# Kernel optimization log

Hardware: AMD Instinct MI355X
Metric: run time of the kernel (lower is better)

Reference implementation:

```python
import jax, jax.numpy as jnp
import numpy as np

TOPK = 16  # module init arg
EPS = 1e-12  # F.normalize eps


def setup_inputs() -> dict:
    key = jax.random.key(0)
    k1, k2, k3 = jax.random.split(key, 3)
    b, c, h, w = 2, 256, 96, 96
    rc = max(c // 4, 16)  # reduced_channels = 64
    x = jax.random.normal(k1, (b, c, h, w), dtype=jnp.float32)
    # 1x1 convs are channel-mixing matmuls; store weights as [out_ch, in_ch]
    w_reduce = jax.random.normal(k2, (rc, c), dtype=jnp.float32) * 0.05
    w_proj = jax.random.normal(k3, (c, rc), dtype=jnp.float32) * 0.05
    return {"x": x, "w_reduce": w_reduce, "w_proj": w_proj}


def reference(x, w_reduce, w_proj):
    b, c, h, w = x.shape
    n = h * w
    # reduce: 1x1 conv == channel matmul -> [b, rc, N]
    feat = jnp.einsum('rc,bchw->brhw', w_reduce, x).reshape(b, -1, n)
    # F.normalize(dim=1): divide by max(L2-norm over channels, eps)
    nrm = jnp.maximum(jnp.sqrt(jnp.sum(feat * feat, axis=1, keepdims=True)), EPS)
    nf = jnp.transpose(feat / nrm, (0, 2, 1))  # [b, N, rc]
    # cosine similarity matrix [b, N, N]
    sim = jnp.einsum('bnr,bmr->bnm', nf, nf)
    k = min(TOPK, n)
    _, idx = jax.lax.top_k(sim, k)  # [b, N, k]
    # gather top-k neighbor features and average -> [b, N, rc]
    corr = jax.vmap(lambda f, i: f[i].mean(axis=1))(nf, idx)
    # proj: 1x1 conv back to C channels, NCHW layout
    enhanced = jnp.einsum('cr,bnr->bnc', w_proj, corr)
    enhanced = jnp.transpose(enhanced, (0, 2, 1)).reshape(b, c, h, w)
    return x + enhanced
```

## Files before the change

### kernel.cpp

```cpp
#include <hip/hip_runtime.h>
#include <cstdint>
#include <cstddef>

#define NPIX 9216
#define NB 2
#define NC 256
#define RC 64
#define TK 16
#define NROWS (NB * NPIX)
#define CT 128
#define ECOLS 1152
#define NTE 9
#define MAXC 128
#define MARGIN 0.008f

typedef unsigned short ushort_t;
typedef unsigned int uint_t;
typedef __bf16 bf16x8 __attribute__((ext_vector_type(8)));
typedef float f32x4 __attribute__((ext_vector_type(4)));

__device__ __forceinline__ uint_t f2bf(float x) {
  uint_t u = __float_as_uint(x);
  return (u + 0x7FFFu + ((u >> 16) & 1u)) >> 16;
}

__device__ __forceinline__ uint_t ordu(float v) {
  uint_t u = __float_as_uint(v);
  return (u & 0x80000000u) ? ~u : (u | 0x80000000u);
}

__global__ __launch_bounds__(256) void k_reduce(
    const float* __restrict__ x, const float* __restrict__ wr,
    float* __restrict__ feat4) {
  __shared__ float wl[64 * 16];
  const int bi = blockIdx.x;
  const int pg = bi >> 4, rq = (bi >> 2) & 3, cq = bi & 3;
  const int tid = threadIdx.x;
  {
    const int cl = tid >> 2, rg = (tid & 3) * 4;
#pragma unroll
    for (int i = 0; i < 4; ++i)
      wl[cl * 16 + rg + i] = wr[(size_t)(rq * 16 + rg + i) * NC + cq * 64 + cl];
  }
  __syncthreads();

  const int p = pg * 256 + tid;
  const int b = p >= NPIX;
  const int n = p - b * NPIX;
  const float* xp = x + (size_t)b * NC * NPIX + (size_t)cq * 64 * NPIX + n;

  float4 acc[4];
#pragma unroll
  for (int i = 0; i < 4; ++i) acc[i] = make_float4(0.f, 0.f, 0.f, 0.f);

  for (int c = 0; c < 64; ++c) {
    const float xv = xp[(size_t)c * NPIX];
    const float4* w4 = (const float4*)(wl + c * 16);
#pragma unroll
    for (int i = 0; i < 4; ++i) {
      float4 w = w4[i];
      acc[i].x += w.x * xv; acc[i].y += w.y * xv;
      acc[i].z += w.z * xv; acc[i].w += w.w * xv;
    }
  }
  float4* o = (float4*)(feat4 + (((size_t)(rq * 4 + cq)) * NROWS + p) * 16);
#pragma unroll
  for (int i = 0; i < 4; ++i) o[i] = acc[i];
}

__global__ __launch_bounds__(256) void k_normsplit(
    const float* __restrict__ feat4, float* __restrict__ nf,
    ushort_t* __restrict__ hi) {
  const int t = blockIdx.x * 256 + threadIdx.x;
  const int p = t >> 2, q = t & 3;
  float4 v[4];
#pragma unroll
  for (int i = 0; i < 4; ++i) v[i] = make_float4(0.f, 0.f, 0.f, 0.f);
#pragma unroll
  for (int pt = 0; pt < 4; ++pt) {
    const float4* fp = (const float4*)(feat4 + (((size_t)(q * 4 + pt)) * NROWS + p) * 16);
#pragma unroll
    for (int i = 0; i < 4; ++i) {
      float4 a = fp[i];
      v[i].x += a.x; v[i].y += a.y; v[i].z += a.z; v[i].w += a.w;
    }
  }
  float ssq = 0.f;
#pragma unroll
  for (int i = 0; i < 4; ++i)
    ssq += v[i].x * v[i].x + v[i].y * v[i].y + v[i].z * v[i].z + v[i].w * v[i].w;
  ssq += __shfl_xor(ssq, 1);
  ssq += __shfl_xor(ssq, 2);
  const float inv = 1.f / fmaxf(sqrtf(ssq), 1e-12f);

  float s[16];
#pragma unroll
  for (int i = 0; i < 4; ++i) {
    s[i * 4 + 0] = v[i].x * inv; s[i * 4 + 1] = v[i].y * inv;
    s[i * 4 + 2] = v[i].z * inv; s[i * 4 + 3] = v[i].w * inv;
  }
  float4* no = (float4*)(nf + (size_t)p * RC + q * 16);
#pragma unroll
  for (int i = 0; i < 4; ++i)
    no[i] = make_float4(s[i * 4], s[i * 4 + 1], s[i * 4 + 2], s[i * 4 + 3]);

  uint_t hs[16];
#pragma unroll
  for (int i = 0; i < 16; ++i) hs[i] = f2bf(s[i]);
  uint4* ho = (uint4*)(hi + (size_t)p * RC + q * 16);
#pragma unroll
  for (int h = 0; h < 2; ++h)
    ho[h] = make_uint4(hs[h*8+0] | (hs[h*8+1] << 16), hs[h*8+2] | (hs[h*8+3] << 16),
                       hs[h*8+4] | (hs[h*8+5] << 16), hs[h*8+6] | (hs[h*8+7] << 16));
}

__global__ __launch_bounds__(256) void k_sim_max(
    const ushort_t* __restrict__ nf_hi, float* __restrict__ tmax) {
  __shared__ ushort_t sh[CT * 72];
  const int rb = blockIdx.x >> 3, q = blockIdx.x & 7;
  const int tid = threadIdx.x, wave = tid >> 6, lane = tid & 63;
  const int n = lane & 15, quad = lane >> 4;
  const int r0 = rb * 128 + wave * 32 + n, r1 = r0 + 16;
  const int b = rb >= 72;
  const size_t cbase = (size_t)b * NPIX;

  const bf16x8 bh00 = *(const bf16x8*)(nf_hi + (size_t)r0 * 64 + quad * 8);
  const bf16x8 bh01 = *(const bf16x8*)(nf_hi + (size_t)r0 * 64 + 32 + quad * 8);
  const bf16x8 bh10 = *(const bf16x8*)(nf_hi + (size_t)r1 * 64 + quad * 8);
  const bf16x8 bh11 = *(const bf16x8*)(nf_hi + (size_t)r1 * 64 + 32 + quad * 8);

  const int sc = tid >> 1, sseg = (tid & 1) * 32;
  float cm0 = -1e30f, cm1 = -1e30f;

  for (int t = 0; t < NTE; ++t) {
    const int cb = q * ECOLS + t * CT;
    __syncthreads();
    {
      const uint4* g = (const uint4*)(nf_hi + (cbase + cb + sc) * 64 + sseg);
      uint4* d = (uint4*)(sh + sc * 72 + sseg);
#pragma unroll
      for (int i = 0; i < 4; ++i) d[i] = g[i];
    }
    __syncthreads();

#pragma unroll 2
    for (int st = 0; st < 8; ++st) {
      const ushort_t* ap = sh + (st * 16 + n) * 72 + quad * 8;
      bf16x8 ah0 = *(const bf16x8*)ap;
      bf16x8 ah1 = *(const bf16x8*)(ap + 32);
      f32x4 z = {0.f, 0.f, 0.f, 0.f};
      f32x4 a0 = __builtin_amdgcn_mfma_f32_16x16x32_bf16(ah0, bh00, z, 0, 0, 0);
      a0 = __builtin_amdgcn_mfma_f32_16x16x32_bf16(ah1, bh01, a0, 0, 0, 0);
      f32x4 a1 = __builtin_amdgcn_mfma_f32_16x16x32_bf16(ah0, bh10, z, 0, 0, 0);
      a1 = __builtin_amdgcn_mfma_f32_16x16x32_bf16(ah1, bh11, a1, 0, 0, 0);
      cm0 = fmaxf(cm0, fmaxf(fmaxf(a0[0], a0[1]), fmaxf(a0[2], a0[3])));
      cm1 = fmaxf(cm1, fmaxf(fmaxf(a1[0], a1[1]), fmaxf(a1[2], a1[3])));
    }
    if (t % 3 == 2) {
      const int cn = t / 3;
      tmax[(size_t)r0 * 96 + (q * 4 + quad) * 3 + cn] = cm0;
      tmax[(size_t)r1 * 96 + (q * 4 + quad) * 3 + cn] = cm1;
      cm0 = -1e30f; cm1 = -1e30f;
    }
  }
}

__global__ __launch_bounds__(256) void k_thresh(
    const float* __restrict__ tmax, float* __restrict__ Tb) {
  const int wave = threadIdx.x >> 6, lane = threadIdx.x & 63;
  const int row = blockIdx.x * 4 + wave;
  const float* tp = tmax + (size_t)row * 96;
  float v0 = tp[lane];
  float v1 = (lane < 32) ? tp[64 + lane] : -1e30f;
  float m = -1e30f;
#pragma unroll
  for (int k = 0; k < TK; ++k) {
    float c = fmaxf(v0, v1);
#pragma unroll
    for (int d = 1; d < 64; d <<= 1) c = fmaxf(c, __shfl_xor(c, d));
    m = c;
    if (v0 == m) v0 = -1e30f;
    if (v1 == m) v1 = -1e30f;
  }
  if (lane == 0) Tb[row] = m - MARGIN;
}

__global__ __launch_bounds__(256) void k_collect(
    const ushort_t* __restrict__ nf_hi, const float* __restrict__ Tb,
    int* __restrict__ cidx, int* __restrict__ rowcnt) {
  __shared__ ushort_t sh[CT * 72];
  const int rb = blockIdx.x >> 3, q = blockIdx.x & 7;
  const int tid = threadIdx.x, wave = tid >> 6, lane = tid & 63;
  const int n = lane & 15, quad = lane >> 4;
  const int r0 = rb * 128 + wave * 32 + n, r1 = r0 + 16;
  const int b = rb >= 72;
  const size_t cbase = (size_t)b * NPIX;

  const bf16x8 bh00 = *(const bf16x8*)(nf_hi + (size_t)r0 * 64 + quad * 8);
  const bf16x8 bh01 = *(const bf16x8*)(nf_hi + (size_t)r0 * 64 + 32 + quad * 8);
  const bf16x8 bh10 = *(const bf16x8*)(nf_hi + (size_t)r1 * 64 + quad * 8);
  const bf16x8 bh11 = *(const bf16x8*)(nf_hi + (size_t)r1 * 64 + 32 + quad * 8);

  const float T0 = Tb[r0], T1 = Tb[r1];
  const int sc = tid >> 1, sseg = (tid & 1) * 32;

  for (int t = 0; t < NTE; ++t) {
    const int cb = q * ECOLS + t * CT;
    __syncthreads();
    {
      const uint4* g = (const uint4*)(nf_hi + (cbase + cb + sc) * 64 + sseg);
      uint4* d = (uint4*)(sh + sc * 72 + sseg);
#pragma unroll
      for (int i = 0; i < 4; ++i) d[i] = g[i];
    }
    __syncthreads();

#pragma unroll 2
    for (int st = 0; st < 8; ++st) {
      const ushort_t* ap = sh + (st * 16 + n) * 72 + quad * 8;
      bf16x8 ah0 = *(const bf16x8*)ap;
      bf16x8 ah1 = *(const bf16x8*)(ap + 32);
      f32x4 z = {0.f, 0.f, 0.f, 0.f};
      f32x4 a0 = __builtin_amdgcn_mfma_f32_16x16x32_bf16(ah0, bh00, z, 0, 0, 0);
      a0 = __builtin_amdgcn_mfma_f32_16x16x32_bf16(ah1, bh01, a0, 0, 0, 0);
      f32x4 a1 = __builtin_amdgcn_mfma_f32_16x16x32_bf16(ah0, bh10, z, 0, 0, 0);
      a1 = __builtin_amdgcn_mfma_f32_16x16x32_bf16(ah1, bh11, a1, 0, 0, 0);

      const int c0 = cb + st * 16 + quad * 4;
      const float mx0 = fmaxf(fmaxf(a0[0], a0[1]), fmaxf(a0[2], a0[3]));
      if (mx0 >= T0) {
#pragma unroll
        for (int r = 0; r < 4; ++r)
          if (a0[r] >= T0) {
            const int slot = atomicAdd(rowcnt + r0, 1);
            if (slot < MAXC) cidx[(size_t)r0 * MAXC + slot] = c0 + r;
          }
      }
      const float mx1 = fmaxf(fmaxf(a1[0], a1[1]), fmaxf(a1[2], a1[3]));
      if (mx1 >= T1) {
#pragma unroll
        for (int r = 0; r < 4; ++r)
          if (a1[r] >= T1) {
            const int slot = atomicAdd(rowcnt + r1, 1);
            if (slot < MAXC) cidx[(size_t)r1 * MAXC + slot] = c0 + r;
          }
      }
    }
  }
}

__global__ __launch_bounds__(256) void k_merge_gather(
    const float* __restrict__ nf, const int* __restrict__ cidx,
    const int* __restrict__ rowcnt, float* __restrict__ corr) {
  const int wave = threadIdx.x >> 6, lane = threadIdx.x & 63;
  const int row0 = blockIdx.x * 16 + wave * 4;
#pragma unroll 1
  for (int rr = 0; rr < 4; ++rr) {
    const int row = row0 + rr;
    const int b = row >= NPIX;
    const int rl = row - b * NPIX;
    const float* nfb = nf + (size_t)b * NPIX * RC;
    const int C = min(rowcnt[row], MAXC);

    float4 rv[16];
    const float4* r4 = (const float4*)(nf + (size_t)row * RC);
#pragma unroll
    for (int i = 0; i < 16; ++i) rv[i] = r4[i];

    const int* cp = cidx + (size_t)row * MAXC;
    unsigned long long k0 = 0, k1 = 0;
    {
      const int c0 = (lane < C) ? cp[lane] : rl;
      const float4* g = (const float4*)(nfb + (size_t)c0 * RC);
      float s = 0.f;
#pragma unroll
      for (int i = 0; i < 16; ++i) {
        float4 a = g[i];
        s += a.x * rv[i].x + a.y * rv[i].y + a.z * rv[i].z + a.w * rv[i].w;
      }
      if (lane < C)
        k0 = ((unsigned long long)ordu(s) << 32) | (uint_t)(~(uint_t)c0);
    }
    if (C > 64) {
      const int c1 = (64 + lane < C) ? cp[64 + lane] : rl;
      const float4* g = (const float4*)(nfb + (size_t)c1 * RC);
      float s = 0.f;
#pragma unroll
      for (int i = 0; i < 16; ++i) {
        float4 a = g[i];
        s += a.x * rv[i].x + a.y * rv[i].y + a.z * rv[i].z + a.w * rv[i].w;
      }
      if (64 + lane < C)
        k1 = ((unsigned long long)ordu(s) << 32) | (uint_t)(~(uint_t)c1);
    }

    int sel[TK];
#pragma unroll
    for (int t = 0; t < TK; ++t) {
      unsigned long long m = k0 > k1 ? k0 : k1;
#pragma unroll
      for (int d = 1; d < 64; d <<= 1) {
        unsigned long long o = __shfl_xor(m, d);
        m = (o > m) ? o : m;
      }
      sel[t] = (m == 0) ? rl : (int)(~(uint_t)(m & 0xFFFFFFFFull));
      if (k0 == m) k0 = 0;
      else if (k1 == m) k1 = 0;
    }

    float acc = 0.f;
#pragma unroll
    for (int t = 0; t < TK; ++t)
      acc += nfb[(size_t)sel[t] * RC + lane];
    corr[(size_t)row * RC + lane] = acc * 0.0625f;
  }
}

__global__ __launch_bounds__(256) void k_proj_add(
    const float* __restrict__ x, const float* __restrict__ wp,
    const float* __restrict__ corr, float* __restrict__ out) {
  const int pg = blockIdx.x >> 3, cq = blockIdx.x & 7;
  const int tid = threadIdx.x;

  __shared__ float wl[32 * RC];
  {
    const float4* src = (const float4*)(wp + (size_t)cq * 32 * RC);
    float4* dst = (float4*)wl;
#pragma unroll
    for (int i = 0; i < 2; ++i) dst[i * 256 + tid] = src[i * 256 + tid];
  }

  const int p = pg * 256 + tid;
  const int b = p >= NPIX;
  const int n = p - b * NPIX;

  float4 cr[16];
  const float4* c4 = (const float4*)(corr + (size_t)p * RC);
#pragma unroll
  for (int i = 0; i < 16; ++i) cr[i] = c4[i];
  __syncthreads();

  const size_t xb = (size_t)b * NC * NPIX + n;
  for (int cl = 0; cl < 32; ++cl) {
    const float4* w4 = (const float4*)(wl + cl * RC);
    float s = 0.f;
#pragma unroll
    for (int i = 0; i < 16; ++i) {
      float4 w = w4[i];
      s += w.x * cr[i].x + w.y * cr[i].y + w.z * cr[i].z + w.w * cr[i].w;
    }
    const int c = cq * 32 + cl;
    const size_t oi = xb + (size_t)c * NPIX;
    out[oi] = x[oi] + s;
  }
}

extern "C" void kernel_launch(void* const* d_in, const int* in_sizes, int n_in,
                              void* d_out, int out_size, void* d_ws, size_t ws_size,
                              hipStream_t stream) {
  const float* x = (const float*)d_in[0];
  const float* wr = (const float*)d_in[1];
  const float* wp = (const float*)d_in[2];
  float* out = (float*)d_out;

  char* ws = (char*)d_ws;
  float* feat4 = (float*)ws;
  float* tmax = (float*)ws;
  float* corr = (float*)ws;
  float* nf = (float*)(ws + 18874368);
  ushort_t* nf_hi = (ushort_t*)(ws + 23592960);
  float* Tb = (float*)(ws + 25952256);
  int* rowcnt = (int*)(ws + 26025984);
  int* cidx = (int*)(ws + 26099712);

  hipLaunchKernelGGL(k_reduce, dim3(1152), dim3(256), 0, stream, x, wr, feat4);
  hipLaunchKernelGGL(k_normsplit, dim3(288), dim3(256), 0, stream, feat4, nf, nf_hi);
  hipLaunchKernelGGL(k_sim_max, dim3(1152), dim3(256), 0, stream, nf_hi, tmax);
  hipLaunchKernelGGL(k_thresh, dim3(NROWS / 4), dim3(256), 0, stream, tmax, Tb);
  hipMemsetAsync(rowcnt, 0, NROWS * sizeof(int), stream);
  hipLaunchKernelGGL(k_collect, dim3(1152), dim3(256), 0, stream,
                     nf_hi, Tb, cidx, rowcnt);
  hipLaunchKernelGGL(k_merge_gather, dim3(1152), dim3(256), 0, stream,
                     nf, cidx, rowcnt, corr);
  hipLaunchKernelGGL(k_proj_add, dim3(576), dim3(256), 0, stream, x, wp, corr, out);
}
```

Baseline: 311.6 us.

## Register-prefetch column tiles, split sim columns 16 ways, widen reduce outputs

The similarity-max and collect kernels now prefetch the next column tile into registers while the current tile is processed from shared memory. Column tiles shrink from 128 to 96 and the column range is split 16 ways instead of 8, doubling the grid to 2304 blocks and producing 128 chunk maxima per row instead of 96. The reduce kernel computes 32 output channels per block instead of 16, halving its grid and the number of x reloads, and normsplit reads the new layout. Together these aim to hide global-load latency behind MFMA work and improve occupancy. The cost is more register pressure and a larger per-row threshold selection over 128 candidates.

```diff
diff --git a/kernel.cpp b/kernel.cpp
--- a/kernel.cpp
+++ b/kernel.cpp
@@ -8,9 +8,12 @@
 #define RC 64
 #define TK 16
 #define NROWS (NB * NPIX)
-#define CT 128
-#define ECOLS 1152
-#define NTE 9
+#define CT 96
+#define SST 72
+#define NQ 16
+#define ECOLS 576
+#define NTE 6
+#define NCHK 128
 #define MAXC 128
 #define MARGIN 0.008f
 
@@ -32,15 +35,15 @@
 __global__ __launch_bounds__(256) void k_reduce(
     const float* __restrict__ x, const float* __restrict__ wr,
     float* __restrict__ feat4) {
-  __shared__ float wl[64 * 16];
+  __shared__ float wl[64 * 32];
   const int bi = blockIdx.x;
-  const int pg = bi >> 4, rq = (bi >> 2) & 3, cq = bi & 3;
+  const int pg = bi >> 3, rh = (bi >> 2) & 1, cq = bi & 3;
   const int tid = threadIdx.x;
   {
-    const int cl = tid >> 2, rg = (tid & 3) * 4;
-#pragma unroll
-    for (int i = 0; i < 4; ++i)
-      wl[cl * 16 + rg + i] = wr[(size_t)(rq * 16 + rg + i) * NC + cq * 64 + cl];
+    const int cl = tid >> 2, rg = (tid & 3) * 8;
+#pragma unroll
+    for (int i = 0; i < 8; ++i)
+      wl[cl * 32 + rg + i] = wr[(size_t)(rh * 32 + rg + i) * NC + cq * 64 + cl];
   }
   __syncthreads();
 
@@ -49,23 +52,23 @@
   const int n = p - b * NPIX;
   const float* xp = x + (size_t)b * NC * NPIX + (size_t)cq * 64 * NPIX + n;
 
-  float4 acc[4];
-#pragma unroll
-  for (int i = 0; i < 4; ++i) acc[i] = make_float4(0.f, 0.f, 0.f, 0.f);
+  float4 acc[8];
+#pragma unroll
+  for (int i = 0; i < 8; ++i) acc[i] = make_float4(0.f, 0.f, 0.f, 0.f);
 
   for (int c = 0; c < 64; ++c) {
     const float xv = xp[(size_t)c * NPIX];
-    const float4* w4 = (const float4*)(wl + c * 16);
-#pragma unroll
-    for (int i = 0; i < 4; ++i) {
+    const float4* w4 = (const float4*)(wl + c * 32);
+#pragma unroll
+    for (int i = 0; i < 8; ++i) {
       float4 w = w4[i];
       acc[i].x += w.x * xv; acc[i].y += w.y * xv;
       acc[i].z += w.z * xv; acc[i].w += w.w * xv;
     }
   }
-  float4* o = (float4*)(feat4 + (((size_t)(rq * 4 + cq)) * NROWS + p) * 16);
-#pragma unroll
-  for (int i = 0; i < 4; ++i) o[i] = acc[i];
+  float4* o = (float4*)(feat4 + (((size_t)(rh * 4 + cq)) * NROWS + p) * 32);
+#pragma unroll
+  for (int i = 0; i < 8; ++i) o[i] = acc[i];
 }
 
 __global__ __launch_bounds__(256) void k_normsplit(
@@ -73,12 +76,13 @@
     ushort_t* __restrict__ hi) {
   const int t = blockIdx.x * 256 + threadIdx.x;
   const int p = t >> 2, q = t & 3;
+  const int rh = q >> 1, so = (q & 1) * 16;
   float4 v[4];
 #pragma unroll
   for (int i = 0; i < 4; ++i) v[i] = make_float4(0.f, 0.f, 0.f, 0.f);
 #pragma unroll
   for (int pt = 0; pt < 4; ++pt) {
-    const float4* fp = (const float4*)(feat4 + (((size_t)(q * 4 + pt)) * NROWS + p) * 16);
+    const float4* fp = (const float4*)(feat4 + (((size_t)(rh * 4 + pt)) * NROWS + p) * 32 + so);
 #pragma unroll
     for (int i = 0; i < 4; ++i) {
       float4 a = fp[i];
@@ -116,8 +120,8 @@
 
 __global__ __launch_bounds__(256) void k_sim_max(
     const ushort_t* __restrict__ nf_hi, float* __restrict__ tmax) {
-  __shared__ ushort_t sh[CT * 72];
-  const int rb = blockIdx.x >> 3, q = blockIdx.x & 7;
+  __shared__ ushort_t sh[CT * SST];
+  const int rb = blockIdx.x >> 4, q = blockIdx.x & 15;
   const int tid = threadIdx.x, wave = tid >> 6, lane = tid & 63;
   const int n = lane & 15, quad = lane >> 4;
   const int r0 = rb * 128 + wave * 32 + n, r1 = r0 + 16;
@@ -129,23 +133,34 @@
   const bf16x8 bh10 = *(const bf16x8*)(nf_hi + (size_t)r1 * 64 + quad * 8);
   const bf16x8 bh11 = *(const bf16x8*)(nf_hi + (size_t)r1 * 64 + 32 + quad * 8);
 
-  const int sc = tid >> 1, sseg = (tid & 1) * 32;
+  const int scol[3] = {tid >> 3, (256 + tid) >> 3, (512 + tid) >> 3};
+  const int soff = (tid & 7) * 8;
+  uint4 rg[3];
+  {
+    const int cb = q * ECOLS;
+#pragma unroll
+    for (int i = 0; i < 3; ++i)
+      rg[i] = *(const uint4*)(nf_hi + (cbase + cb + scol[i]) * 64 + soff);
+  }
+
   float cm0 = -1e30f, cm1 = -1e30f;
 
   for (int t = 0; t < NTE; ++t) {
-    const int cb = q * ECOLS + t * CT;
     __syncthreads();
-    {
-      const uint4* g = (const uint4*)(nf_hi + (cbase + cb + sc) * 64 + sseg);
-      uint4* d = (uint4*)(sh + sc * 72 + sseg);
-#pragma unroll
-      for (int i = 0; i < 4; ++i) d[i] = g[i];
+#pragma unroll
+    for (int i = 0; i < 3; ++i)
+      *(uint4*)(sh + scol[i] * SST + soff) = rg[i];
+    if (t + 1 < NTE) {
+      const int cb = q * ECOLS + (t + 1) * CT;
+#pragma unroll
+      for (int i = 0; i < 3; ++i)
+        rg[i] = *(const uint4*)(nf_hi + (cbase + cb + scol[i]) * 64 + soff);
     }
     __syncthreads();
 
 #pragma unroll 2
-    for (int st = 0; st < 8; ++st) {
-      const ushort_t* ap = sh + (st * 16 + n) * 72 + quad * 8;
+    for (int st = 0; st < 6; ++st) {
+      const ushort_t* ap = sh + (st * 16 + n) * SST + quad * 8;
       bf16x8 ah0 = *(const bf16x8*)ap;
       bf16x8 ah1 = *(const bf16x8*)(ap + 32);
       f32x4 z = {0.f, 0.f, 0.f, 0.f};
@@ -156,10 +171,10 @@
       cm0 = fmaxf(cm0, fmaxf(fmaxf(a0[0], a0[1]), fmaxf(a0[2], a0[3])));
       cm1 = fmaxf(cm1, fmaxf(fmaxf(a1[0], a1[1]), fmaxf(a1[2], a1[3])));
     }
-    if (t % 3 == 2) {
-      const int cn = t / 3;
-      tmax[(size_t)r0 * 96 + (q * 4 + quad) * 3 + cn] = cm0;
-      tmax[(size_t)r1 * 96 + (q * 4 + quad) * 3 + cn] = cm1;
+    if (t == 2 || t == 5) {
+      const int cn = (q * 4 + quad) * 2 + (t / 3);
+      tmax[(size_t)r0 * NCHK + cn] = cm0;
+      tmax[(size_t)r1 * NCHK + cn] = cm1;
       cm0 = -1e30f; cm1 = -1e30f;
     }
   }
@@ -169,9 +184,9 @@
     const float* __restrict__ tmax, float* __restrict__ Tb) {
   const int wave = threadIdx.x >> 6, lane = threadIdx.x & 63;
   const int row = blockIdx.x * 4 + wave;
-  const float* tp = tmax + (size_t)row * 96;
+  const float* tp = tmax + (size_t)row * NCHK;
   float v0 = tp[lane];
-  float v1 = (lane < 32) ? tp[64 + lane] : -1e30f;
+  float v1 = tp[64 + lane];
   float m = -1e30f;
 #pragma unroll
   for (int k = 0; k < TK; ++k) {
@@ -188,8 +203,8 @@
 __global__ __launch_bounds__(256) void k_collect(
     const ushort_t* __restrict__ nf_hi, const float* __restrict__ Tb,
     int* __restrict__ cidx, int* __restrict__ rowcnt) {
-  __shared__ ushort_t sh[CT * 72];
-  const int rb = blockIdx.x >> 3, q = blockIdx.x & 7;
+  __shared__ ushort_t sh[CT * SST];
+  const int rb = blockIdx.x >> 4, q = blockIdx.x & 15;
   const int tid = threadIdx.x, wave = tid >> 6, lane = tid & 63;
   const int n = lane & 15, quad = lane >> 4;
   const int r0 = rb * 128 + wave * 32 + n, r1 = r0 + 16;
@@ -202,22 +217,34 @@
   const bf16x8 bh11 = *(const bf16x8*)(nf_hi + (size_t)r1 * 64 + 32 + quad * 8);
 
   const float T0 = Tb[r0], T1 = Tb[r1];
-  const int sc = tid >> 1, sseg = (tid & 1) * 32;
+
+  const int scol[3] = {tid >> 3, (256 + tid) >> 3, (512 + tid) >> 3};
+  const int soff = (tid & 7) * 8;
+  uint4 rg[3];
+  {
+    const int cb = q * ECOLS;
+#pragma unroll
+    for (int i = 0; i < 3; ++i)
+      rg[i] = *(const uint4*)(nf_hi + (cbase + cb + scol[i]) * 64 + soff);
+  }
 
   for (int t = 0; t < NTE; ++t) {
     const int cb = q * ECOLS + t * CT;
     __syncthreads();
-    {
-      const uint4* g = (const uint4*)(nf_hi + (cbase + cb + sc) * 64 + sseg);
-      uint4* d = (uint4*)(sh + sc * 72 + sseg);
-#pragma unroll
-      for (int i = 0; i < 4; ++i) d[i] = g[i];
+#pragma unroll
+    for (int i = 0; i < 3; ++i)
+      *(uint4*)(sh + scol[i] * SST + soff) = rg[i];
+    if (t + 1 < NTE) {
+      const int cb1 = q * ECOLS + (t + 1) * CT;
+#pragma unroll
+      for (int i = 0; i < 3; ++i)
+        rg[i] = *(const uint4*)(nf_hi + (cbase + cb1 + scol[i]) * 64 + soff);
     }
     __syncthreads();
 
 #pragma unroll 2
-    for (int st = 0; st < 8; ++st) {
-      const ushort_t* ap = sh + (st * 16 + n) * 72 + quad * 8;
+    for (int st = 0; st < 6; ++st) {
+      const ushort_t* ap = sh + (st * 16 + n) * SST + quad * 8;
       bf16x8 ah0 = *(const bf16x8*)ap;
       bf16x8 ah1 = *(const bf16x8*)(ap + 32);
       f32x4 z = {0.f, 0.f, 0.f, 0.f};
@@ -373,12 +400,12 @@
   int* rowcnt = (int*)(ws + 26025984);
   int* cidx = (int*)(ws + 26099712);
 
-  hipLaunchKernelGGL(k_reduce, dim3(1152), dim3(256), 0, stream, x, wr, feat4);
+  hipLaunchKernelGGL(k_reduce, dim3(576), dim3(256), 0, stream, x, wr, feat4);
   hipLaunchKernelGGL(k_normsplit, dim3(288), dim3(256), 0, stream, feat4, nf, nf_hi);
-  hipLaunchKernelGGL(k_sim_max, dim3(1152), dim3(256), 0, stream, nf_hi, tmax);
+  hipLaunchKernelGGL(k_sim_max, dim3(2304), dim3(256), 0, stream, nf_hi, tmax);
   hipLaunchKernelGGL(k_thresh, dim3(NROWS / 4), dim3(256), 0, stream, tmax, Tb);
   hipMemsetAsync(rowcnt, 0, NROWS * sizeof(int), stream);
-  hipLaunchKernelGGL(k_collect, dim3(1152), dim3(256), 0, stream,
+  hipLaunchKernelGGL(k_collect, dim3(2304), dim3(256), 0, stream,
                      nf_hi, Tb, cidx, rowcnt);
   hipLaunchKernelGGL(k_merge_gather, dim3(1152), dim3(256), 0, stream,
                      nf, cidx, rowcnt, corr);
```

Measured after the change: 370.2 us. 1.19x slower.
